# Performance work log

Measured on AMD Instinct MI355X. Metric: run time of the kernel, lower is better.

The kernel has to match this reference:

```python
import jax, jax.numpy as jnp
import numpy as np

N = 50000        # nodes
E = 600000       # edges
F_IN = 128       # num_node_features
H = 128          # hidden_channels
G = 2000         # number of graphs (batch segments)
C = 1            # num_classes
EPS = 1e-5       # BatchNorm eps


def setup_inputs() -> dict:
    key = jax.random.key(0)
    ks = jax.random.split(key, 12)
    x = jax.random.normal(ks[0], (N, F_IN), dtype=jnp.float32)
    edge_index = jax.random.randint(ks[1], (2, E), 0, N, dtype=jnp.int32)
    batch = jnp.sort(jax.random.randint(ks[2], (N,), 0, G, dtype=jnp.int32))
    s = 0.05
    W1 = jax.random.normal(ks[3], (F_IN, H), dtype=jnp.float32) * s
    b1 = jnp.zeros((H,), dtype=jnp.float32)
    W2 = jax.random.normal(ks[4], (H, H), dtype=jnp.float32) * s
    b2 = jnp.zeros((H,), dtype=jnp.float32)
    W3 = jax.random.normal(ks[5], (H, H), dtype=jnp.float32) * s
    b3 = jnp.zeros((H,), dtype=jnp.float32)
    # BatchNorm (eval mode): running stats + affine params, stacked [3, H]
    bn_gamma = jnp.ones((3, H), dtype=jnp.float32)
    bn_beta = jnp.zeros((3, H), dtype=jnp.float32)
    bn_mean = jnp.zeros((3, H), dtype=jnp.float32)
    bn_var = jnp.ones((3, H), dtype=jnp.float32)
    lin1_W = jax.random.normal(ks[6], (3 * H, H), dtype=jnp.float32) * s
    lin1_b = jnp.zeros((H,), dtype=jnp.float32)
    lin2_W = jax.random.normal(ks[7], (H, C), dtype=jnp.float32) * s
    lin2_b = jnp.zeros((C,), dtype=jnp.float32)
    return {"x": x, "edge_index": edge_index, "batch": batch,
            "W1": W1, "b1": b1, "W2": W2, "b2": b2, "W3": W3, "b3": b3,
            "bn_gamma": bn_gamma, "bn_beta": bn_beta, "bn_mean": bn_mean, "bn_var": bn_var,
            "lin1_W": lin1_W, "lin1_b": lin1_b, "lin2_W": lin2_W, "lin2_b": lin2_b}


def _gcn_norm(edge_index):
    # Add self loops, compute symmetric normalization D^-1/2 (A+I) D^-1/2.
    loop = jnp.arange(N, dtype=edge_index.dtype)
    row = jnp.concatenate([edge_index[0], loop])   # sources (E+N,)
    col = jnp.concatenate([edge_index[1], loop])   # targets (E+N,)
    deg = jax.ops.segment_sum(jnp.ones(E + N, dtype=jnp.float32), col, num_segments=N)
    dinv = jnp.where(deg > 0, jax.lax.rsqrt(deg), 0.0)
    norm = dinv[row] * dinv[col]                   # (E+N,)
    return row, col, norm


def _gcn_conv(h, W, b, row, col, norm):
    h = h @ W                                      # [N, H] transform first (PyG GCNConv)
    msg = h[row] * norm[:, None]                   # edge-wise gather + scale
    out = jax.ops.segment_sum(msg, col, num_segments=N)  # scatter-add aggregate
    return out + b


def _bn_relu(h, g, b, m, v):
    return jax.nn.relu((h - m) * jax.lax.rsqrt(v + EPS) * g + b)


def reference(x, edge_index, batch, W1, b1, W2, b2, W3, b3,
              bn_gamma, bn_beta, bn_mean, bn_var,
              lin1_W, lin1_b, lin2_W, lin2_b):
    row, col, norm = _gcn_norm(edge_index)
    h = _bn_relu(_gcn_conv(x, W1, b1, row, col, norm), bn_gamma[0], bn_beta[0], bn_mean[0], bn_var[0])
    h = _bn_relu(_gcn_conv(h, W2, b2, row, col, norm), bn_gamma[1], bn_beta[1], bn_mean[1], bn_var[1])
    h = _bn_relu(_gcn_conv(h, W3, b3, row, col, norm), bn_gamma[2], bn_beta[2], bn_mean[2], bn_var[2])
    # Multi-pool over ragged graph segments
    seg = batch
    x_sum = jax.ops.segment_sum(h, seg, num_segments=G)                 # [G, H]
    cnt = jax.ops.segment_sum(jnp.ones((N,), dtype=h.dtype), seg, num_segments=G)
    x_mean = x_sum / jnp.maximum(cnt, 1.0)[:, None]
    x_max = jax.ops.segment_max(h, seg, num_segments=G)
    x_max = jnp.where(jnp.isfinite(x_max), x_max, 0.0)                  # empty segments -> 0
    z = jnp.concatenate([x_mean, x_max, x_sum], axis=1)                 # [G, 3H]
    z = jax.nn.relu(z @ lin1_W + lin1_b)
    return z @ lin2_W + lin2_b                                          # [G, C]
```

## Files before the change

kernel.cpp:

```cpp
#include <hip/hip_runtime.h>
#include <cfloat>
#include <cstdint>

#define N_NODES 50000
#define N_EDGES 600000
#define HDIM    128
#define NGRAPH  2000
#define BN_EPS  1e-5f


__global__ void k_init(int* degi, int* seg_s, int* seg_e) {
    int i = blockIdx.x * 256 + threadIdx.x;
    if (i < N_NODES) degi[i] = 1;
    if (i < NGRAPH) { seg_s[i] = 0x7FFFFFFF; seg_e[i] = 0; }
}

__global__ void k_count(const int* __restrict__ ei, int* degi) {
    int e = blockIdx.x * 256 + threadIdx.x;
    if (e < N_EDGES) atomicAdd(&degi[ei[N_EDGES + e]], 1);
}

__global__ void k_dinv(const int* __restrict__ degi, float* dinv) {
    int i = blockIdx.x * 256 + threadIdx.x;
    if (i < N_NODES) dinv[i] = rsqrtf((float)degi[i]);
}

__global__ void k_scanA(const int* __restrict__ degi, int* ptr, int* bsum) {
    __shared__ int t[256];
    int i = blockIdx.x * 256 + threadIdx.x;
    int v = (i < N_NODES) ? degi[i] : 0;
    t[threadIdx.x] = v; __syncthreads();
    for (int off = 1; off < 256; off <<= 1) {
        int a = (threadIdx.x >= off) ? t[threadIdx.x - off] : 0;
        __syncthreads();
        t[threadIdx.x] += a;
        __syncthreads();
    }
    if (i < N_NODES) ptr[i + 1] = t[threadIdx.x];
    if (threadIdx.x == 255) bsum[blockIdx.x] = t[255];
}

__global__ void k_scanB(const int* __restrict__ bsum, int* boff, int nb) {
    __shared__ int t[256];
    int i = threadIdx.x;
    int v = (i < nb) ? bsum[i] : 0;
    t[i] = v; __syncthreads();
    for (int off = 1; off < 256; off <<= 1) {
        int a = (i >= off) ? t[i - off] : 0;
        __syncthreads();
        t[i] += a;
        __syncthreads();
    }
    if (i < nb) boff[i] = t[i] - v;
}

__global__ void k_scanC(int* ptr, const int* __restrict__ boff, int* cursor) {
    int i = blockIdx.x * 256 + threadIdx.x;
    if (i < N_NODES) {
        int val = ptr[i + 1] + boff[blockIdx.x];
        ptr[i + 1] = val;
        if (i + 1 < N_NODES) cursor[i + 1] = val;
    }
    if (i == 0) { ptr[0] = 0; cursor[0] = 0; }
}

__global__ void k_fill(const int* __restrict__ ei, const float* __restrict__ dinv,
                       int* cursor, int2* meta) {
    int e = blockIdx.x * 256 + threadIdx.x;
    if (e < N_EDGES) {
        int r = ei[e], c = ei[N_EDGES + e];
        int pos = atomicAdd(&cursor[c], 1);
        meta[pos] = make_int2(r, __float_as_int(dinv[r] * dinv[c]));
    } else if (e < N_EDGES + N_NODES) {
        int v = e - N_EDGES;
        int pos = atomicAdd(&cursor[v], 1);
        float d = dinv[v];
        meta[pos] = make_int2(v, __float_as_int(d * d));
    }
}

__global__ void k_seg(const int* __restrict__ batch, int* seg_s, int* seg_e) {
    int i = blockIdx.x * 256 + threadIdx.x;
    if (i < N_NODES) {
        int g = batch[i];
        atomicMin(&seg_s[g], i);
        atomicMax(&seg_e[g], i + 1);
    }
}


__global__ __launch_bounds__(256) void k_transform(const float4* __restrict__ hin4,
                                                   const float4* __restrict__ W4,
                                                   float4* __restrict__ hout4) {
    __shared__ float4 Hs[32 * 32];
    size_t g4 = (size_t)blockIdx.x * 1024;
#pragma unroll
    for (int p = 0; p < 4; p++) {
        int idx = threadIdx.x + p * 256;
        if (g4 + idx < (size_t)N_NODES * 32) Hs[idx] = hin4[g4 + idx];
    }
    __syncthreads();

    int ct = threadIdx.x & 31;
    int nt = threadIdx.x >> 5;
    int base = blockIdx.x * 32;

    float4 acc0 = make_float4(0.f, 0.f, 0.f, 0.f);
    float4 acc1 = acc0, acc2 = acc0, acc3 = acc0;

#pragma unroll 4
    for (int kc = 0; kc < 32; kc++) {
        float4 ha = Hs[(nt * 4 + 0) * 32 + kc];
        float4 hb = Hs[(nt * 4 + 1) * 32 + kc];
        float4 hc = Hs[(nt * 4 + 2) * 32 + kc];
        float4 hd = Hs[(nt * 4 + 3) * 32 + kc];
        float4 w0 = W4[(kc * 4 + 0) * 32 + ct];
        float4 w1 = W4[(kc * 4 + 1) * 32 + ct];
        float4 w2 = W4[(kc * 4 + 2) * 32 + ct];
        float4 w3 = W4[(kc * 4 + 3) * 32 + ct];

        acc0.x += ha.x * w0.x + ha.y * w1.x + ha.z * w2.x + ha.w * w3.x;
        acc0.y += ha.x * w0.y + ha.y * w1.y + ha.z * w2.y + ha.w * w3.y;
        acc0.z += ha.x * w0.z + ha.y * w1.z + ha.z * w2.z + ha.w * w3.z;
        acc0.w += ha.x * w0.w + ha.y * w1.w + ha.z * w2.w + ha.w * w3.w;

        acc1.x += hb.x * w0.x + hb.y * w1.x + hb.z * w2.x + hb.w * w3.x;
        acc1.y += hb.x * w0.y + hb.y * w1.y + hb.z * w2.y + hb.w * w3.y;
        acc1.z += hb.x * w0.z + hb.y * w1.z + hb.z * w2.z + hb.w * w3.z;
        acc1.w += hb.x * w0.w + hb.y * w1.w + hb.z * w2.w + hb.w * w3.w;

        acc2.x += hc.x * w0.x + hc.y * w1.x + hc.z * w2.x + hc.w * w3.x;
        acc2.y += hc.x * w0.y + hc.y * w1.y + hc.z * w2.y + hc.w * w3.y;
        acc2.z += hc.x * w0.z + hc.y * w1.z + hc.z * w2.z + hc.w * w3.z;
        acc2.w += hc.x * w0.w + hc.y * w1.w + hc.z * w2.w + hc.w * w3.w;

        acc3.x += hd.x * w0.x + hd.y * w1.x + hd.z * w2.x + hd.w * w3.x;
        acc3.y += hd.x * w0.y + hd.y * w1.y + hd.z * w2.y + hd.w * w3.y;
        acc3.z += hd.x * w0.z + hd.y * w1.z + hd.z * w2.z + hd.w * w3.z;
        acc3.w += hd.x * w0.w + hd.y * w1.w + hd.z * w2.w + hd.w * w3.w;
    }

    int n0 = base + nt * 4;
    if (n0 + 0 < N_NODES) hout4[(size_t)(n0 + 0) * 32 + ct] = acc0;
    if (n0 + 1 < N_NODES) hout4[(size_t)(n0 + 1) * 32 + ct] = acc1;
    if (n0 + 2 < N_NODES) hout4[(size_t)(n0 + 2) * 32 + ct] = acc2;
    if (n0 + 3 < N_NODES) hout4[(size_t)(n0 + 3) * 32 + ct] = acc3;
}


__global__ __launch_bounds__(256) void k_aggregate(const float4* __restrict__ h4,
                                                   const int* __restrict__ ptr,
                                                   const int2* __restrict__ meta,
                                                   const float4* __restrict__ bias4,
                                                   const float4* __restrict__ bng4,
                                                   const float4* __restrict__ bnb4,
                                                   const float4* __restrict__ bnm4,
                                                   const float4* __restrict__ bnv4,
                                                   float4* __restrict__ hout4) {
    int v = blockIdx.x * 8 + (threadIdx.x >> 5);
    int c = threadIdx.x & 31;
    if (v >= N_NODES) return;
    int e0 = ptr[v], e1 = ptr[v + 1];

    float ax = 0.f, ay = 0.f, az = 0.f, aw = 0.f;
    int j = e0;
    for (; j + 4 <= e1; j += 4) {
        int2 m0 = meta[j], m1 = meta[j + 1], m2 = meta[j + 2], m3 = meta[j + 3];
        float4 v0 = h4[(size_t)m0.x * 32 + c];
        float4 v1 = h4[(size_t)m1.x * 32 + c];
        float4 v2 = h4[(size_t)m2.x * 32 + c];
        float4 v3 = h4[(size_t)m3.x * 32 + c];
        float n0 = __int_as_float(m0.y), n1 = __int_as_float(m1.y);
        float n2 = __int_as_float(m2.y), n3 = __int_as_float(m3.y);
        ax += n0 * v0.x + n1 * v1.x + n2 * v2.x + n3 * v3.x;
        ay += n0 * v0.y + n1 * v1.y + n2 * v2.y + n3 * v3.y;
        az += n0 * v0.z + n1 * v1.z + n2 * v2.z + n3 * v3.z;
        aw += n0 * v0.w + n1 * v1.w + n2 * v2.w + n3 * v3.w;
    }
    int rem = e1 - j;
    if (rem > 0) {
        int i1 = j + (rem > 1 ? 1 : 0);
        int i2 = j + (rem > 2 ? 2 : 0);
        int2 m0 = meta[j], m1 = meta[i1], m2 = meta[i2];
        float4 v0 = h4[(size_t)m0.x * 32 + c];
        float4 v1 = h4[(size_t)m1.x * 32 + c];
        float4 v2 = h4[(size_t)m2.x * 32 + c];
        float n0 = __int_as_float(m0.y);
        float n1 = (rem > 1) ? __int_as_float(m1.y) : 0.f;
        float n2 = (rem > 2) ? __int_as_float(m2.y) : 0.f;
        ax += n0 * v0.x + n1 * v1.x + n2 * v2.x;
        ay += n0 * v0.y + n1 * v1.y + n2 * v2.y;
        az += n0 * v0.z + n1 * v1.z + n2 * v2.z;
        aw += n0 * v0.w + n1 * v1.w + n2 * v2.w;
    }

    float4 bs = bias4[c], g = bng4[c], bb = bnb4[c], m = bnm4[c], vv = bnv4[c];
    float sx = g.x * rsqrtf(vv.x + BN_EPS), tx = bb.x - m.x * sx;
    float sy = g.y * rsqrtf(vv.y + BN_EPS), ty = bb.y - m.y * sy;
    float sz = g.z * rsqrtf(vv.z + BN_EPS), tz = bb.z - m.z * sz;
    float sw = g.w * rsqrtf(vv.w + BN_EPS), tw = bb.w - m.w * sw;
    float4 r;
    r.x = fmaxf((ax + bs.x) * sx + tx, 0.f);
    r.y = fmaxf((ay + bs.y) * sy + ty, 0.f);
    r.z = fmaxf((az + bs.z) * sz + tz, 0.f);
    r.w = fmaxf((aw + bs.w) * sw + tw, 0.f);
    hout4[(size_t)v * 32 + c] = r;
}


__global__ __launch_bounds__(128) void k_pool(const float* __restrict__ h,
                                              const int* __restrict__ seg_s,
                                              const int* __restrict__ seg_e,
                                              const float* __restrict__ l1W,
                                              const float* __restrict__ l1b,
                                              const float* __restrict__ l2W,
                                              const float* __restrict__ l2b,
                                              float* __restrict__ out) {
    __shared__ float z[3 * HDIM];
    __shared__ float red[2];
    int g = blockIdx.x, c = threadIdx.x;
    int s = seg_s[g], e = seg_e[g];
    float sum = 0.f, mx = -FLT_MAX;
    for (int i = s; i < e; i++) {
        float val = h[(size_t)i * HDIM + c];
        sum += val;
        mx = fmaxf(mx, val);
    }
    int cnt = (s < e) ? (e - s) : 0;
    if (cnt == 0) { mx = 0.f; sum = 0.f; }
    float mean = sum / (float)(cnt > 1 ? cnt : 1);
    z[c] = mean; z[HDIM + c] = mx; z[2 * HDIM + c] = sum;
    __syncthreads();
    float o = l1b[c];
    for (int k = 0; k < 3 * HDIM; k++) o += z[k] * l1W[k * HDIM + c];
    o = fmaxf(o, 0.f);
    float p = o * l2W[c];
#pragma unroll
    for (int off = 32; off; off >>= 1) p += __shfl_down(p, off, 64);
    if ((c & 63) == 0) red[c >> 6] = p;
    __syncthreads();
    if (c == 0) out[g] = red[0] + red[1] + l2b[0];
}


extern "C" void kernel_launch(void* const* d_in, const int* in_sizes, int n_in,
                              void* d_out, int out_size, void* d_ws, size_t ws_size,
                              hipStream_t stream) {
    const float* x   = (const float*)d_in[0];
    const int*   ei  = (const int*)d_in[1];
    const int*   bat = (const int*)d_in[2];
    const float* W1  = (const float*)d_in[3];
    const float* b1  = (const float*)d_in[4];
    const float* W2  = (const float*)d_in[5];
    const float* b2  = (const float*)d_in[6];
    const float* W3  = (const float*)d_in[7];
    const float* b3  = (const float*)d_in[8];
    const float* bng = (const float*)d_in[9];
    const float* bnb = (const float*)d_in[10];
    const float* bnm = (const float*)d_in[11];
    const float* bnv = (const float*)d_in[12];
    const float* l1W = (const float*)d_in[13];
    const float* l1b = (const float*)d_in[14];
    const float* l2W = (const float*)d_in[15];
    const float* l2b = (const float*)d_in[16];
    float* out = (float*)d_out;

    char* ws = (char*)d_ws;
    size_t off = 0;
    auto alloc = [&](size_t bytes) -> char* {
        char* p = ws + off;
        off = (off + bytes + 255) & ~(size_t)255;
        return p;
    };
    int*   degi   = (int*)alloc((size_t)N_NODES * 4);
    float* dinv   = (float*)alloc((size_t)N_NODES * 4);
    int*   ptr    = (int*)alloc((size_t)(N_NODES + 1) * 4);
    int*   cursor = (int*)alloc((size_t)N_NODES * 4);
    int*   bsum   = (int*)alloc(256 * 4);
    int*   boff   = (int*)alloc(256 * 4);
    int*   seg_s  = (int*)alloc((size_t)NGRAPH * 4);
    int*   seg_e  = (int*)alloc((size_t)NGRAPH * 4);
    int2*  meta   = (int2*)alloc((size_t)(N_EDGES + N_NODES) * 8);
    float* hA     = (float*)alloc((size_t)N_NODES * HDIM * 4);
    float* hB     = (float*)alloc((size_t)N_NODES * HDIM * 4);
    (void)ws_size;

    int nblk = (N_NODES + 255) / 256;

    k_init<<<nblk, 256, 0, stream>>>(degi, seg_s, seg_e);
    k_count<<<(N_EDGES + 255) / 256, 256, 0, stream>>>(ei, degi);
    k_dinv<<<nblk, 256, 0, stream>>>(degi, dinv);
    k_scanA<<<nblk, 256, 0, stream>>>(degi, ptr, bsum);
    k_scanB<<<1, 256, 0, stream>>>(bsum, boff, nblk);
    k_scanC<<<nblk, 256, 0, stream>>>(ptr, boff, cursor);
    k_fill<<<(N_EDGES + N_NODES + 255) / 256, 256, 0, stream>>>(ei, dinv, cursor, meta);
    k_seg<<<nblk, 256, 0, stream>>>(bat, seg_s, seg_e);

    int tb = (N_NODES + 31) / 32;
    int ab = (N_NODES + 7) / 8;

    k_transform<<<tb, 256, 0, stream>>>((const float4*)x, (const float4*)W1, (float4*)hA);
    k_aggregate<<<ab, 256, 0, stream>>>((const float4*)hA, ptr, meta, (const float4*)b1,
                                        (const float4*)(bng + 0), (const float4*)(bnb + 0),
                                        (const float4*)(bnm + 0), (const float4*)(bnv + 0),
                                        (float4*)hB);
    k_transform<<<tb, 256, 0, stream>>>((const float4*)hB, (const float4*)W2, (float4*)hA);
    k_aggregate<<<ab, 256, 0, stream>>>((const float4*)hA, ptr, meta, (const float4*)b2,
                                        (const float4*)(bng + HDIM), (const float4*)(bnb + HDIM),
                                        (const float4*)(bnm + HDIM), (const float4*)(bnv + HDIM),
                                        (float4*)hB);
    k_transform<<<tb, 256, 0, stream>>>((const float4*)hB, (const float4*)W3, (float4*)hA);
    k_aggregate<<<ab, 256, 0, stream>>>((const float4*)hA, ptr, meta, (const float4*)b3,
                                        (const float4*)(bng + 2 * HDIM), (const float4*)(bnb + 2 * HDIM),
                                        (const float4*)(bnm + 2 * HDIM), (const float4*)(bnv + 2 * HDIM),
                                        (float4*)hB);

    k_pool<<<NGRAPH, 128, 0, stream>>>(hB, seg_s, seg_e, l1W, l1b, l2W, l2b, out);
}
```

Baseline: 350.8 us.

## Fuse aggregation and transform per layer by reordering to aggregate-then-multiply

Uses linearity (A·(hW) = (A·h)W) to aggregate neighbor features first into shared memory and then apply the weight matrix, bias, BatchNorm and ReLU in one kernel per layer. This removes the intermediate N×128 write and read between transform and aggregate, and halves the layer kernel launches. It also folds the dinv computation into the scan kernel and unrolls the gather loop to 8 edges. In exchange, nodes with low in-degree waste lanes because the remainder is padded to 8, and per-block gather latency is now serialized before the matmul.

```diff
diff --git a/kernel.cpp b/kernel.cpp
--- a/kernel.cpp
+++ b/kernel.cpp
@@ -20,15 +20,11 @@
     if (e < N_EDGES) atomicAdd(&degi[ei[N_EDGES + e]], 1);
 }
 
-__global__ void k_dinv(const int* __restrict__ degi, float* dinv) {
-    int i = blockIdx.x * 256 + threadIdx.x;
-    if (i < N_NODES) dinv[i] = rsqrtf((float)degi[i]);
-}
-
-__global__ void k_scanA(const int* __restrict__ degi, int* ptr, int* bsum) {
+__global__ void k_scanA(const int* __restrict__ degi, int* ptr, int* bsum, float* dinv) {
     __shared__ int t[256];
     int i = blockIdx.x * 256 + threadIdx.x;
     int v = (i < N_NODES) ? degi[i] : 0;
+    if (i < N_NODES) dinv[i] = rsqrtf((float)v);
     t[threadIdx.x] = v; __syncthreads();
     for (int off = 1; off < 256; off <<= 1) {
         int a = (threadIdx.x >= off) ? t[threadIdx.x - off] : 0;
@@ -89,21 +85,65 @@
 }
 
 
-__global__ __launch_bounds__(256) void k_transform(const float4* __restrict__ hin4,
-                                                   const float4* __restrict__ W4,
-                                                   float4* __restrict__ hout4) {
+__global__ __launch_bounds__(256) void k_layer(const float4* __restrict__ h4,
+                                               const int* __restrict__ ptr,
+                                               const int2* __restrict__ meta,
+                                               const float4* __restrict__ W4,
+                                               const float4* __restrict__ bias4,
+                                               const float4* __restrict__ bng4,
+                                               const float4* __restrict__ bnb4,
+                                               const float4* __restrict__ bnm4,
+                                               const float4* __restrict__ bnv4,
+                                               float4* __restrict__ hout4) {
     __shared__ float4 Hs[32 * 32];
-    size_t g4 = (size_t)blockIdx.x * 1024;
-#pragma unroll
-    for (int p = 0; p < 4; p++) {
-        int idx = threadIdx.x + p * 256;
-        if (g4 + idx < (size_t)N_NODES * 32) Hs[idx] = hin4[g4 + idx];
+    int base = blockIdx.x * 32;
+    int c = threadIdx.x & 31;
+    int grp = threadIdx.x >> 5;
+
+#pragma unroll
+    for (int pass = 0; pass < 4; pass++) {
+        int ln = pass * 8 + grp;
+        int v = base + ln;
+        if (v < N_NODES) {
+            int e0 = ptr[v], e1 = ptr[v + 1];
+            float ax = 0.f, ay = 0.f, az = 0.f, aw = 0.f;
+            int j = e0;
+            for (; j + 8 <= e1; j += 8) {
+                int2 m[8];
+#pragma unroll
+                for (int i = 0; i < 8; i++) m[i] = meta[j + i];
+                float4 vv[8];
+#pragma unroll
+                for (int i = 0; i < 8; i++) vv[i] = h4[(size_t)m[i].x * 32 + c];
+#pragma unroll
+                for (int i = 0; i < 8; i++) {
+                    float n = __int_as_float(m[i].y);
+                    ax += n * vv[i].x; ay += n * vv[i].y;
+                    az += n * vv[i].z; aw += n * vv[i].w;
+                }
+            }
+            int rem = e1 - j;
+            if (rem) {
+                int2 m[8];
+#pragma unroll
+                for (int i = 0; i < 8; i++) m[i] = meta[j + (i < rem ? i : 0)];
+                float4 vv[8];
+#pragma unroll
+                for (int i = 0; i < 8; i++) vv[i] = h4[(size_t)m[i].x * 32 + c];
+#pragma unroll
+                for (int i = 0; i < 8; i++) {
+                    float n = (i < rem) ? __int_as_float(m[i].y) : 0.f;
+                    ax += n * vv[i].x; ay += n * vv[i].y;
+                    az += n * vv[i].z; aw += n * vv[i].w;
+                }
+            }
+            Hs[ln * 32 + c] = make_float4(ax, ay, az, aw);
+        }
     }
     __syncthreads();
 
     int ct = threadIdx.x & 31;
     int nt = threadIdx.x >> 5;
-    int base = blockIdx.x * 32;
 
     float4 acc0 = make_float4(0.f, 0.f, 0.f, 0.f);
     float4 acc1 = acc0, acc2 = acc0, acc3 = acc0;
@@ -140,71 +180,26 @@
         acc3.w += hd.x * w0.w + hd.y * w1.w + hd.z * w2.w + hd.w * w3.w;
     }
 
-    int n0 = base + nt * 4;
-    if (n0 + 0 < N_NODES) hout4[(size_t)(n0 + 0) * 32 + ct] = acc0;
-    if (n0 + 1 < N_NODES) hout4[(size_t)(n0 + 1) * 32 + ct] = acc1;
-    if (n0 + 2 < N_NODES) hout4[(size_t)(n0 + 2) * 32 + ct] = acc2;
-    if (n0 + 3 < N_NODES) hout4[(size_t)(n0 + 3) * 32 + ct] = acc3;
-}
-
-
-__global__ __launch_bounds__(256) void k_aggregate(const float4* __restrict__ h4,
-                                                   const int* __restrict__ ptr,
-                                                   const int2* __restrict__ meta,
-                                                   const float4* __restrict__ bias4,
-                                                   const float4* __restrict__ bng4,
-                                                   const float4* __restrict__ bnb4,
-                                                   const float4* __restrict__ bnm4,
-                                                   const float4* __restrict__ bnv4,
-                                                   float4* __restrict__ hout4) {
-    int v = blockIdx.x * 8 + (threadIdx.x >> 5);
-    int c = threadIdx.x & 31;
-    if (v >= N_NODES) return;
-    int e0 = ptr[v], e1 = ptr[v + 1];
-
-    float ax = 0.f, ay = 0.f, az = 0.f, aw = 0.f;
-    int j = e0;
-    for (; j + 4 <= e1; j += 4) {
-        int2 m0 = meta[j], m1 = meta[j + 1], m2 = meta[j + 2], m3 = meta[j + 3];
-        float4 v0 = h4[(size_t)m0.x * 32 + c];
-        float4 v1 = h4[(size_t)m1.x * 32 + c];
-        float4 v2 = h4[(size_t)m2.x * 32 + c];
-        float4 v3 = h4[(size_t)m3.x * 32 + c];
-        float n0 = __int_as_float(m0.y), n1 = __int_as_float(m1.y);
-        float n2 = __int_as_float(m2.y), n3 = __int_as_float(m3.y);
-        ax += n0 * v0.x + n1 * v1.x + n2 * v2.x + n3 * v3.x;
-        ay += n0 * v0.y + n1 * v1.y + n2 * v2.y + n3 * v3.y;
-        az += n0 * v0.z + n1 * v1.z + n2 * v2.z + n3 * v3.z;
-        aw += n0 * v0.w + n1 * v1.w + n2 * v2.w + n3 * v3.w;
-    }
-    int rem = e1 - j;
-    if (rem > 0) {
-        int i1 = j + (rem > 1 ? 1 : 0);
-        int i2 = j + (rem > 2 ? 2 : 0);
-        int2 m0 = meta[j], m1 = meta[i1], m2 = meta[i2];
-        float4 v0 = h4[(size_t)m0.x * 32 + c];
-        float4 v1 = h4[(size_t)m1.x * 32 + c];
-        float4 v2 = h4[(size_t)m2.x * 32 + c];
-        float n0 = __int_as_float(m0.y);
-        float n1 = (rem > 1) ? __int_as_float(m1.y) : 0.f;
-        float n2 = (rem > 2) ? __int_as_float(m2.y) : 0.f;
-        ax += n0 * v0.x + n1 * v1.x + n2 * v2.x;
-        ay += n0 * v0.y + n1 * v1.y + n2 * v2.y;
-        az += n0 * v0.z + n1 * v1.z + n2 * v2.z;
-        aw += n0 * v0.w + n1 * v1.w + n2 * v2.w;
-    }
-
-    float4 bs = bias4[c], g = bng4[c], bb = bnb4[c], m = bnm4[c], vv = bnv4[c];
+    float4 bs = bias4[ct], g = bng4[ct], bb = bnb4[ct], m = bnm4[ct], vv = bnv4[ct];
     float sx = g.x * rsqrtf(vv.x + BN_EPS), tx = bb.x - m.x * sx;
     float sy = g.y * rsqrtf(vv.y + BN_EPS), ty = bb.y - m.y * sy;
     float sz = g.z * rsqrtf(vv.z + BN_EPS), tz = bb.z - m.z * sz;
     float sw = g.w * rsqrtf(vv.w + BN_EPS), tw = bb.w - m.w * sw;
-    float4 r;
-    r.x = fmaxf((ax + bs.x) * sx + tx, 0.f);
-    r.y = fmaxf((ay + bs.y) * sy + ty, 0.f);
-    r.z = fmaxf((az + bs.z) * sz + tz, 0.f);
-    r.w = fmaxf((aw + bs.w) * sw + tw, 0.f);
-    hout4[(size_t)v * 32 + c] = r;
+
+    int n0 = base + nt * 4;
+    float4 accs[4] = {acc0, acc1, acc2, acc3};
+#pragma unroll
+    for (int q = 0; q < 4; q++) {
+        int nidx = n0 + q;
+        if (nidx < N_NODES) {
+            float4 a = accs[q], r;
+            r.x = fmaxf((a.x + bs.x) * sx + tx, 0.f);
+            r.y = fmaxf((a.y + bs.y) * sy + ty, 0.f);
+            r.z = fmaxf((a.z + bs.z) * sz + tz, 0.f);
+            r.w = fmaxf((a.w + bs.w) * sw + tw, 0.f);
+            hout4[(size_t)nidx * 32 + ct] = r;
+        }
+    }
 }
 
 
@@ -289,31 +284,29 @@
 
     k_init<<<nblk, 256, 0, stream>>>(degi, seg_s, seg_e);
     k_count<<<(N_EDGES + 255) / 256, 256, 0, stream>>>(ei, degi);
-    k_dinv<<<nblk, 256, 0, stream>>>(degi, dinv);
-    k_scanA<<<nblk, 256, 0, stream>>>(degi, ptr, bsum);
+    k_scanA<<<nblk, 256, 0, stream>>>(degi, ptr, bsum, dinv);
     k_scanB<<<1, 256, 0, stream>>>(bsum, boff, nblk);
     k_scanC<<<nblk, 256, 0, stream>>>(ptr, boff, cursor);
     k_fill<<<(N_EDGES + N_NODES + 255) / 256, 256, 0, stream>>>(ei, dinv, cursor, meta);
     k_seg<<<nblk, 256, 0, stream>>>(bat, seg_s, seg_e);
 
-    int tb = (N_NODES + 31) / 32;
-    int ab = (N_NODES + 7) / 8;
-
-    k_transform<<<tb, 256, 0, stream>>>((const float4*)x, (const float4*)W1, (float4*)hA);
-    k_aggregate<<<ab, 256, 0, stream>>>((const float4*)hA, ptr, meta, (const float4*)b1,
-                                        (const float4*)(bng + 0), (const float4*)(bnb + 0),
-                                        (const float4*)(bnm + 0), (const float4*)(bnv + 0),
-                                        (float4*)hB);
-    k_transform<<<tb, 256, 0, stream>>>((const float4*)hB, (const float4*)W2, (float4*)hA);
-    k_aggregate<<<ab, 256, 0, stream>>>((const float4*)hA, ptr, meta, (const float4*)b2,
-                                        (const float4*)(bng + HDIM), (const float4*)(bnb + HDIM),
-                                        (const float4*)(bnm + HDIM), (const float4*)(bnv + HDIM),
-                                        (float4*)hB);
-    k_transform<<<tb, 256, 0, stream>>>((const float4*)hB, (const float4*)W3, (float4*)hA);
-    k_aggregate<<<ab, 256, 0, stream>>>((const float4*)hA, ptr, meta, (const float4*)b3,
-                                        (const float4*)(bng + 2 * HDIM), (const float4*)(bnb + 2 * HDIM),
-                                        (const float4*)(bnm + 2 * HDIM), (const float4*)(bnv + 2 * HDIM),
-                                        (float4*)hB);
-
-    k_pool<<<NGRAPH, 128, 0, stream>>>(hB, seg_s, seg_e, l1W, l1b, l2W, l2b, out);
-}
+    int lb = (N_NODES + 31) / 32;
+
+    k_layer<<<lb, 256, 0, stream>>>((const float4*)x, ptr, meta, (const float4*)W1,
+                                    (const float4*)b1,
+                                    (const float4*)(bng + 0), (const float4*)(bnb + 0),
+                                    (const float4*)(bnm + 0), (const float4*)(bnv + 0),
+                                    (float4*)hA);
+    k_layer<<<lb, 256, 0, stream>>>((const float4*)hA, ptr, meta, (const float4*)W2,
+                                    (const float4*)b2,
+                                    (const float4*)(bng + HDIM), (const float4*)(bnb + HDIM),
+                                    (const float4*)(bnm + HDIM), (const float4*)(bnv + HDIM),
+                                    (float4*)hB);
+    k_layer<<<lb, 256, 0, stream>>>((const float4*)hB, ptr, meta, (const float4*)W3,
+                                    (const float4*)b3,
+                                    (const float4*)(bng + 2 * HDIM), (const float4*)(bnb + 2 * HDIM),
+                                    (const float4*)(bnm + 2 * HDIM), (const float4*)(bnv + 2 * HDIM),
+                                    (float4*)hA);
+
+    k_pool<<<NGRAPH, 128, 0, stream>>>(hA, seg_s, seg_e, l1W, l1b, l2W, l2b, out);
+}
```

Result: faster. 326.5 us (-6.9%).
